# Kernel optimization log

Measured on AMD Instinct MI355X. Metric: run time of the kernel, lower is better.

## Reference

```python
import jax, jax.numpy as jnp
import numpy as np

B, S, D = 4, 2048, 1024
H, HD = 16, 64  # n_heads, head_dim (n_kv_heads == n_heads -> n_rep = 1)
WINDOW = 256
ROPE_THETA = 10000.0


def setup_inputs() -> dict:
    key = jax.random.key(0)
    ks = jax.random.split(key, 5)
    x = jax.random.normal(ks[0], (B, S, D), dtype=jnp.float32)
    scale = 0.02
    wq = jax.random.normal(ks[1], (D, D), dtype=jnp.float32) * scale
    wk = jax.random.normal(ks[2], (D, D), dtype=jnp.float32) * scale
    wv = jax.random.normal(ks[3], (D, D), dtype=jnp.float32) * scale
    wo = jax.random.normal(ks[4], (D, D), dtype=jnp.float32) * scale
    # RoPE frequencies: freqs_cis[t, i] = exp(1j * t / theta^(2i/HD)), i in [0, HD/2)
    inv_freq = 1.0 / (ROPE_THETA ** (jnp.arange(0, HD, 2, dtype=jnp.float32) / HD))
    t = jnp.arange(S, dtype=jnp.float32)
    ang = t[:, None] * inv_freq[None, :]  # [S, HD/2]
    return {"x": x, "freqs_cos": jnp.cos(ang), "freqs_sin": jnp.sin(ang),
            "wq": wq, "wk": wk, "wv": wv, "wo": wo}


def _apply_rope(xq, xk, cos, sin):
    # xq/xk: [B, S, H, HD]; cos/sin: [S, HD/2] broadcast as [1, S, 1, HD/2]
    def rot(v):
        vr = v.reshape(*v.shape[:-1], HD // 2, 2)
        v0, v1 = vr[..., 0], vr[..., 1]
        c = cos[None, :, None, :]
        s = sin[None, :, None, :]
        o0 = v0 * c - v1 * s
        o1 = v0 * s + v1 * c
        return jnp.stack([o0, o1], axis=-1).reshape(v.shape)
    return rot(xq), rot(xk)


def reference(x, freqs_cos, freqs_sin, wq, wk, wv, wo):
    b, s, _ = x.shape
    xq = (x @ wq.T).reshape(b, s, H, HD)
    xk = (x @ wk.T).reshape(b, s, H, HD)
    xv = (x @ wv.T).reshape(b, s, H, HD)
    xq, xk = _apply_rope(xq, xk, freqs_cos, freqs_sin)
    # [B, H, S, S] scores
    scores = jnp.einsum('bqhd,bkhd->bhqk', xq, xk) / jnp.sqrt(jnp.float32(HD))
    pos = jnp.arange(s)
    # masked (disallowed) when j > i (future) or i - j >= window
    bad = (pos[None, :] > pos[:, None]) | (pos[:, None] - pos[None, :] >= WINDOW)
    scores = jnp.where(bad[None, None], -jnp.inf, scores)
    attn = jax.nn.softmax(scores.astype(jnp.float32), axis=-1).astype(xq.dtype)
    out = jnp.einsum('bhqk,bkhd->bqhd', attn, xv).reshape(b, s, H * HD)
    return out @ wo.T
```

## Files before the change

kernel.cpp:

```cpp
#include <hip/hip_runtime.h>
#include <hip/hip_bf16.h>


typedef __bf16 bf16_t;
typedef __attribute__((ext_vector_type(8))) __bf16 bf16x8;
typedef __attribute__((ext_vector_type(4))) __bf16 bf16x4;
typedef __attribute__((ext_vector_type(4))) float f32x4;

#define MFMA16(a, b, c) __builtin_amdgcn_mfma_f32_16x16x32_bf16((a), (b), (c), 0, 0, 0)

__device__ __forceinline__ void async16(const void* g, void* l) {
    __builtin_amdgcn_global_load_lds(
        (const __attribute__((address_space(1))) unsigned int*)g,
        (__attribute__((address_space(3))) unsigned int*)l, 16, 0, 0);
}

#define BAR() do { asm volatile("" ::: "memory"); __builtin_amdgcn_s_barrier(); \
                   asm volatile("" ::: "memory"); } while (0)
#define VMC(N) asm volatile("s_waitcnt vmcnt(" #N ")" ::: "memory")
#define LGKM0() asm volatile("s_waitcnt lgkmcnt(0)" ::: "memory")

__global__ __launch_bounds__(256) void cvt_all(const float* __restrict__ x,
                                               const float* __restrict__ wq,
                                               const float* __restrict__ wk,
                                               const float* __restrict__ wv,
                                               const float* __restrict__ wo,
                                               const float* __restrict__ fcos,
                                               const float* __restrict__ fsin,
                                               bf16_t* __restrict__ xbf,
                                               bf16_t* __restrict__ wqkv,
                                               bf16_t* __restrict__ wobf,
                                               float* __restrict__ fcosT,
                                               float* __restrict__ fsinT) {
    const int blk = blockIdx.x;
    if (blk >= 6144) {
        const int p = blk - 6144;
        for (int s = threadIdx.x; s < 2048; s += 256) {
            fcosT[p * 2048 + s] = fcos[s * 32 + p];
            fsinT[p * 2048 + s] = fsin[s * 32 + p];
        }
        return;
    }
    const float* s;
    bf16_t* d;
    int base;
    if (blk < 4096)      { s = x;  d = xbf;            base = blk; }
    else if (blk < 4608) { s = wq; d = wqkv;           base = blk - 4096; }
    else if (blk < 5120) { s = wk; d = wqkv + 1048576; base = blk - 4608; }
    else if (blk < 5632) { s = wv; d = wqkv + 2097152; base = blk - 5120; }
    else                 { s = wo; d = wobf;           base = blk - 5632; }
    const int i = (base * 256 + threadIdx.x) * 8;
    float4 a = *(const float4*)(s + i);
    float4 b = *(const float4*)(s + i + 4);
    bf16x8 o;
    o[0] = (bf16_t)a.x; o[1] = (bf16_t)a.y; o[2] = (bf16_t)a.z; o[3] = (bf16_t)a.w;
    o[4] = (bf16_t)b.x; o[5] = (bf16_t)b.y; o[6] = (bf16_t)b.z; o[7] = (bf16_t)b.w;
    *(bf16x8*)(d + i) = o;
}

__global__ __launch_bounds__(512, 1) __attribute__((amdgpu_waves_per_eu(2)))
void gemm192_qkv(const bf16_t* __restrict__ A, const bf16_t* __restrict__ Bw,
                 const float* __restrict__ fcosT, const float* __restrict__ fsinT,
                 bf16_t* __restrict__ Qo, bf16_t* __restrict__ Ko,
                 bf16_t* __restrict__ VT, int M, int N, int K) {
    __shared__ __attribute__((aligned(16))) bf16_t As[32768];
    __shared__ __attribute__((aligned(16))) bf16_t Bs[24576];
    const int tid = threadIdx.x;
    const int l = tid & 63, w = tid >> 6;
    const int lr = l & 15, lg = l >> 4;
    const int wr = w >> 2, wc = w & 3;

    const int nwg = gridDim.x * gridDim.y;
    const int flat = blockIdx.y * gridDim.x + blockIdx.x;
    const int swz = (flat & 7) * (nwg >> 3) + (flat >> 3);
    const int bx = swz % gridDim.x, by = swz / gridDim.x;
    const long m0 = (long)by * 256, n0 = (long)bx * 192;
    const int NT = K >> 6;
    const int NI = NT >> 1;

    const int p  = w * 1024 + l * 16;
    const int pp = p ^ (((p >> 9) & 1) << 5);
    const int st = pp >> 10;
    const int rSt = (st >> 1) * 16 + ((pp >> 6) & 15);
    const int cSt = (st & 1) * 32 + ((pp >> 4) & 3) * 8;
    const bf16_t* aS = A  + (m0 + rSt) * K + cSt;
    const bf16_t* bS = Bw + (n0 + rSt) * K + cSt;
    const long uK = 64L * K;

    auto stageA = [&](int b, int u, int t) {
        async16(aS + (long)u * uK + (long)t * 64,
                (char*)As + b * 32768 + u * 8192 + w * 1024);
    };
    auto stageB = [&](int b, int u, int t) {
        async16(bS + (long)u * uK + (long)t * 64,
                (char*)Bs + b * 24576 + u * 8192 + w * 1024);
    };

    f32x4 acc[8][3] = {};
    bf16x8 afX[4], afY[4], bfX[3], bfY[3];
    const int swd = (lr & 8) << 2;

    auto loadAF = [&](int b, int mh, int ks, bf16x8 (&dst)[4]) {
#pragma unroll
        for (int mi = 0; mi < 4; ++mi) {
            const int off = (wr * 2 + mh) * 8192 + (mi * 2 + ks) * 1024 +
                            lr * 64 + lg * 16;
            dst[mi] = *(const bf16x8*)((const char*)As + b * 32768 + (off ^ swd));
        }
    };
    auto loadBF = [&](int b, int ks, bf16x8 (&dst)[3]) {
#pragma unroll
        for (int nj = 0; nj < 3; ++nj) {
            const int rg = wc * 48 + nj * 16 + lr;
            const int off = (rg >> 6) * 8192 + (((rg >> 4) & 3) * 2 + ks) * 1024 +
                            lr * 64 + lg * 16;
            dst[nj] = *(const bf16x8*)((const char*)Bs + b * 24576 + (off ^ swd));
        }
    };

#define QMM(MH, AF, BF) do {                                                   \
    __builtin_amdgcn_s_setprio(1);                                             \
    _Pragma("unroll")                                                          \
    for (int mi = 0; mi < 4; ++mi)                                             \
        _Pragma("unroll")                                                      \
        for (int nj = 0; nj < 3; ++nj)                                         \
            acc[(MH)*4+mi][nj] = MFMA16((AF)[mi], (BF)[nj], acc[(MH)*4+mi][nj]); \
    __builtin_amdgcn_s_setprio(0);                                             \
} while (0)

    stageA(0, 0, 0); stageA(0, 1, 0); stageA(0, 2, 0); stageA(0, 3, 0);
    stageB(0, 0, 0); stageB(0, 1, 0); stageB(0, 2, 0);
    stageB(1, 0, 1); stageB(1, 1, 1); stageB(1, 2, 1);
    VMC(3);
    BAR();

#pragma unroll 1
    for (int it = 0; it < NI - 1; ++it) {
        const int T = 2 * it;
        loadAF(0, 0, 0, afX); loadBF(0, 0, bfX);
        stageA(1, 0, T + 1); stageA(1, 1, T + 1);
        BAR(); QMM(0, afX, bfX); BAR();
        loadAF(0, 1, 0, afY);
        stageA(1, 2, T + 1); stageA(1, 3, T + 1);
        BAR(); QMM(1, afY, bfX); BAR();
        loadAF(0, 0, 1, afX); loadBF(0, 1, bfY);
        BAR(); QMM(0, afX, bfY); BAR();
        loadAF(0, 1, 1, afY);
        stageB(0, 0, T + 2);
        BAR(); QMM(1, afY, bfY); VMC(1); BAR();
        loadAF(1, 0, 0, afX); loadBF(1, 0, bfX);
        stageB(0, 1, T + 2); stageB(0, 2, T + 2);
        BAR(); QMM(0, afX, bfX); BAR();
        loadAF(1, 1, 0, afY);
        stageA(0, 0, T + 2); stageA(0, 1, T + 2);
        BAR(); QMM(1, afY, bfX); BAR();
        loadAF(1, 0, 1, afX); loadBF(1, 1, bfY);
        stageA(0, 2, T + 2); stageA(0, 3, T + 2);
        BAR(); QMM(0, afX, bfY); BAR();
        loadAF(1, 1, 1, afY);
        stageB(1, 0, T + 3); stageB(1, 1, T + 3); stageB(1, 2, T + 3);
        BAR(); QMM(1, afY, bfY); VMC(3); BAR();
    }

    {
        loadAF(0, 0, 0, afX); loadBF(0, 0, bfX);
        stageA(1, 0, NT - 1); stageA(1, 1, NT - 1);
        BAR(); QMM(0, afX, bfX); BAR();
        loadAF(0, 1, 0, afY);
        stageA(1, 2, NT - 1); stageA(1, 3, NT - 1);
        BAR(); QMM(1, afY, bfX); BAR();
        loadAF(0, 0, 1, afX); loadBF(0, 1, bfY);
        BAR(); QMM(0, afX, bfY); BAR();
        loadAF(0, 1, 1, afY);
        BAR(); QMM(1, afY, bfY);
        VMC(0); BAR();
        loadAF(1, 0, 0, afX); loadBF(1, 0, bfX);
        QMM(0, afX, bfX);
        loadAF(1, 1, 0, afY);
        QMM(1, afY, bfX);
        loadAF(1, 0, 1, afX); loadBF(1, 1, bfY);
        QMM(0, afX, bfY);
        loadAF(1, 1, 1, afY);
        QMM(1, afY, bfY);
    }
#undef QMM

    bf16_t* scr = (w < 6) ? (bf16_t*)((char*)As + w * 4608)
                          : (bf16_t*)((char*)Bs + (w - 6) * 4608);
    asm volatile("" ::: "memory");

#pragma unroll
    for (int nj = 0; nj < 3; ++nj) {
        const int cbase = (int)n0 + wc * 48 + nj * 16;
        const int cls = cbase >> 10;
        if (cls == 2) {
#pragma unroll
            for (int ai = 0; ai < 8; ++ai)
#pragma unroll
                for (int j = 0; j < 4; ++j)
                    scr[(ai * 16 + lg * 4 + j) * 18 + lr] = (bf16_t)acc[ai][nj][j];
            LGKM0();
            asm volatile("" ::: "memory");
            const int ch = l & 15;
            const int g0 = l >> 4;
            const int d16 = cbase - 2048 + ch;
            const int hh = d16 >> 6, dd = d16 & 63;
            const long T0 = m0 + wr * 128;
            const int bb = (int)(T0 >> 11);
            const int s0 = (int)(T0 & 2047);
            bf16_t* vrow = VT + ((long)((bb * 16 + hh) * 64 + dd) * 2048) + s0;
#pragma unroll
            for (int qq = 0; qq < 4; ++qq) {
                const int grp = g0 + qq * 4;
                bf16x8 o;
#pragma unroll
                for (int j = 0; j < 8; ++j) {
                    const int f = ((j & 3) << 1) | (j >> 2);
                    o[j] = scr[(grp * 8 + f) * 18 + ch];
                }
                *(bf16x8*)(vrow + grp * 8) = o;
            }
            LGKM0();
            asm volatile("" ::: "memory");
        } else {
            const int c = cbase + lr;
            const int dd = c & 63;
            const int p2 = dd >> 1;
            const int hh = (c >> 6) & 15;
            const float sgn = (lr & 1) ? 1.f : -1.f;
            bf16_t* qk = (cls == 0) ? Qo : Ko;
            const float* cT = fcosT + p2 * 2048;
            const float* sT = fsinT + p2 * 2048;
#pragma unroll
            for (int ai = 0; ai < 8; ++ai) {
                const long t0 = m0 + wr * 128 + ai * 16 + lg * 4;
                const int s0 = (int)(t0 & 2047);
                const int bb = (int)(t0 >> 11);
                const float4 cc = *(const float4*)(cT + s0);
                const float4 ss = *(const float4*)(sT + s0);
                bf16_t* row = qk + ((long)(bb * 16 + hh) * 2048 + s0) * 64 + dd;
                const float v0 = acc[ai][nj][0], pv0 = __shfl_xor(acc[ai][nj][0], 1);
                const float v1 = acc[ai][nj][1], pv1 = __shfl_xor(acc[ai][nj][1], 1);
                const float v2 = acc[ai][nj][2], pv2 = __shfl_xor(acc[ai][nj][2], 1);
                const float v3 = acc[ai][nj][3], pv3 = __shfl_xor(acc[ai][nj][3], 1);
                row[0]       = (bf16_t)(v0 * cc.x + sgn * (pv0 * ss.x));
                row[64]      = (bf16_t)(v1 * cc.y + sgn * (pv1 * ss.y));
                row[128]     = (bf16_t)(v2 * cc.z + sgn * (pv2 * ss.z));
                row[192]     = (bf16_t)(v3 * cc.w + sgn * (pv3 * ss.w));
            }
        }
    }
}

template <typename OUT>
__global__ __launch_bounds__(512, 2) void gemm256(const bf16_t* __restrict__ A,
                                                  const bf16_t* __restrict__ Bw,
                                                  OUT* __restrict__ C,
                                                  int M, int N, int K) {
    __shared__ __attribute__((aligned(16))) bf16_t As[49152];
    __shared__ __attribute__((aligned(16))) bf16_t Bs[24576];
    const int tid = threadIdx.x;
    const int l = tid & 63, w = tid >> 6;
    const int lr = l & 15, lg = l >> 4;
    const int wr = w >> 1, wc = w & 1;

    const int nwg = gridDim.x * gridDim.y;
    const int flat = blockIdx.y * gridDim.x + blockIdx.x;
    const int swz = (flat & 7) * (nwg >> 3) + (flat >> 3);
    const int bx = swz % gridDim.x, by = swz / gridDim.x;
    const long m0 = (long)by * 256, n0 = (long)bx * 128;
    const int NT = K >> 6;

    int rS[2], cS[2];
#pragma unroll
    for (int i = 0; i < 2; ++i) {
        const int p  = i * 8192 + w * 1024 + l * 16;
        const int pp = p ^ (((p >> 9) & 1) << 5);
        const int st = pp >> 10;
        rS[i] = (st >> 1) * 16 + ((pp >> 6) & 15);
        cS[i] = (st & 1) * 32 + ((pp >> 4) & 3) * 8;
    }
    const bf16_t* aSrc0 = A  + (m0 + rS[0]) * K + cS[0];
    const bf16_t* aSrc1 = A  + (m0 + rS[1]) * K + cS[1];
    const bf16_t* bSrc0 = Bw + (n0 + rS[0]) * K + cS[0];
    const bf16_t* bSrc1 = Bw + (n0 + rS[1]) * K + cS[1];
    const long hK = 128L * K;

    auto stageA = [&](int b, int h, int t) {
        char* d = (char*)As + b * 32768 + h * 16384 + w * 1024;
        const long o = (long)h * hK + (long)t * 64;
        async16(aSrc0 + o, d);
        async16(aSrc1 + o, d + 8192);
    };
    auto stageB = [&](int b, int t) {
        char* d = (char*)Bs + b * 16384 + w * 1024;
        const long o = (long)t * 64;
        async16(bSrc0 + o, d);
        async16(bSrc1 + o, d + 8192);
    };

    f32x4 acc[4][4] = {};
    bf16x8 af[4][2], blo[2][2], bhi[2][2];
    const int swd = (lr & 8) << 2;

    auto loadA = [&](int b) {
#pragma unroll
        for (int mi = 0; mi < 4; ++mi)
#pragma unroll
            for (int ks = 0; ks < 2; ++ks) {
                const int ra = (wr & 1) * 64 + mi * 16 + lr;
                const int off = ((ra >> 4) * 2 + ks) * 1024 + (ra & 15) * 64 + lg * 16;
                af[mi][ks] = *(const bf16x8*)((const char*)As + b * 32768 +
                                              (wr >> 1) * 16384 + (off ^ swd));
            }
    };
    auto loadB = [&](int b, int nh, bf16x8 (&dst)[2][2]) {
#pragma unroll
        for (int nj = 0; nj < 2; ++nj)
#pragma unroll
            for (int ks = 0; ks < 2; ++ks) {
                const int rb = wc * 64 + (nh * 2 + nj) * 16 + lr;
                const int off = ((rb >> 4) * 2 + ks) * 1024 + (rb & 15) * 64 + lg * 16;
                dst[nj][ks] = *(const bf16x8*)((const char*)Bs + b * 16384 +
                                               (off ^ swd));
            }
    };

#define QMM(NH, BF) do {                                                       \
    __builtin_amdgcn_s_setprio(1);                                             \
    _Pragma("unroll")                                                          \
    for (int mi = 0; mi < 4; ++mi) {                                           \
        acc[mi][(NH)*2]   = MFMA16(af[mi][0], (BF)[0][0], acc[mi][(NH)*2]);    \
        acc[mi][(NH)*2]   = MFMA16(af[mi][1], (BF)[0][1], acc[mi][(NH)*2]);    \
        acc[mi][(NH)*2+1] = MFMA16(af[mi][0], (BF)[1][0], acc[mi][(NH)*2+1]);  \
        acc[mi][(NH)*2+1] = MFMA16(af[mi][1], (BF)[1][1], acc[mi][(NH)*2+1]);  \
    }                                                                          \
    __builtin_amdgcn_s_setprio(0);                                             \
} while (0)

    stageA(0, 0, 0); stageA(0, 1, 0); stageB(0, 0);
    stageA(1, 0, 1); stageA(1, 1, 1); stageB(1, 1);
    VMC(6);
    BAR();

    int bc = 0;
#pragma unroll 1
    for (int t = 0; t < NT - 2; ++t) {
        const int bn = (bc + 2 >= 3) ? bc - 1 : bc + 2;
        loadA(bc); loadB(bc, 0, blo); stageA(bn, 0, t + 2); stageA(bn, 1, t + 2);
        BAR(); QMM(0, blo); BAR();
        loadB(bc, 1, bhi); stageB(bn, t + 2);
        BAR(); QMM(1, bhi);
        if (t < NT - 3) { VMC(6); } else { VMC(0); }
        BAR();
        bc = (bc + 1 >= 3) ? 0 : bc + 1;
    }
    {
        loadA(bc); loadB(bc, 0, blo);
        QMM(0, blo);
        loadB(bc, 1, bhi);
        QMM(1, bhi);
        const int b2 = (bc + 1 >= 3) ? 0 : bc + 1;
        loadA(b2); loadB(b2, 0, blo);
        QMM(0, blo);
        loadB(b2, 1, bhi);
        QMM(1, bhi);
    }
#undef QMM

#pragma unroll
    for (int mi = 0; mi < 4; ++mi)
#pragma unroll
        for (int ni = 0; ni < 4; ++ni)
#pragma unroll
            for (int j = 0; j < 4; ++j) {
                long r = m0 + wr * 64 + mi * 16 + lg * 4 + j;
                long c = n0 + wc * 64 + ni * 16 + lr;
                C[r * N + c] = (OUT)acc[mi][ni][j];
            }
}

__global__ __launch_bounds__(256, 2) void attn_win4(const bf16_t* __restrict__ Q,
                                                    const bf16_t* __restrict__ Kb,
                                                    const bf16_t* __restrict__ VT,
                                                    bf16_t* __restrict__ Ao) {
    __shared__ __attribute__((aligned(16))) bf16_t kld[5 * 4096];
    __shared__ __attribute__((aligned(16))) bf16_t vld[5 * 4096];
    const int raw = blockIdx.x;
    const int mswz = ((raw & 7) << 8) | (raw >> 3);
    const int qt = mswz & 31, bh = mswz >> 5;
    const int h = bh & 15, b = bh >> 4;
    const int l = threadIdx.x & 63, w = threadIdx.x >> 6;
    const int lr = l & 15, lg = l >> 4;
    const int q0 = qt * 64 + w * 16;
    const int q = q0 + lr;
    const int tb = qt - 4;

    const bf16_t* Qp = Q + (long)bh * 2048 * 64;
    const bf16_t* Kp = Kb + (long)bh * 2048 * 64;
    const bf16_t* Vp = VT + (long)bh * 64 * 2048;

#pragma unroll
    for (int u = 0; u < 5; ++u) {
        const int kt = tb + u;
        const int kt64 = (kt < 0 ? 0 : kt) * 64;
#pragma unroll
        for (int part = 0; part < 2; ++part) {
            const int seg = w * 2 + part;
            const int r = seg * 8 + (l >> 3);
            const int sc = (l & 7) ^ ((r >> 1) & 7);
            async16(Kp + (long)(kt64 + r) * 64 + sc * 8,
                    (char*)kld + u * 8192 + seg * 1024);
            async16(Vp + (long)r * 2048 + kt64 + sc * 8,
                    (char*)vld + u * 8192 + seg * 1024);
        }
    }

    const bf16x8 qb0 = *(const bf16x8*)&Qp[q * 64 + lg * 8];
    const bf16x8 qb1 = *(const bf16x8*)&Qp[q * 64 + 32 + lg * 8];

    __syncthreads();

    float mrun = -1000.f, lsum = 0.f;
    f32x4 o0 = {0.f, 0.f, 0.f, 0.f}, o1 = {0.f, 0.f, 0.f, 0.f};
    f32x4 o2 = {0.f, 0.f, 0.f, 0.f}, o3 = {0.f, 0.f, 0.f, 0.f};
    const int swv = (lr >> 1) & 7;

    const char* kbase;
    const char* vbase;
    int k0s;

#define QKCORE(HH, MM)                                                           \
        const int row_ = (HH) * 32 + 2 * lr + (MM);                              \
        const int sw_ = (row_ >> 1) & 7;                                         \
        bf16x8 k0_ = *(const bf16x8*)(kbase + row_ * 128 + ((lg ^ sw_) << 4));   \
        bf16x8 k1_ = *(const bf16x8*)(kbase + row_ * 128 + (((4 + lg) ^ sw_) << 4)); \
        f32x4 s_ = {0.f, 0.f, 0.f, 0.f};                                         \
        s_ = MFMA16(k0_, qb0, s_);                                               \
        s_ = MFMA16(k1_, qb1, s_);

#define QKF_F(DST, HH, MM)                                                       \
    f32x4 DST; { QKCORE(HH, MM)                                                  \
        const int kb_ = k0s + (HH) * 32 + (MM) + lg * 8;                         \
        DST[0] = ((kb_ >= 0) & ((unsigned)(q - kb_) < 256u))         ? s_[0] * 0.125f : -1e30f; \
        DST[1] = ((kb_ + 2 >= 0) & ((unsigned)(q - kb_ - 2) < 256u)) ? s_[1] * 0.125f : -1e30f; \
        DST[2] = ((kb_ + 4 >= 0) & ((unsigned)(q - kb_ - 4) < 256u)) ? s_[2] * 0.125f : -1e30f; \
        DST[3] = ((kb_ + 6 >= 0) & ((unsigned)(q - kb_ - 6) < 256u)) ? s_[3] * 0.125f : -1e30f; \
    }

#define QKF_U(DST, HH, MM)                                                       \
    f32x4 DST; { QKCORE(HH, MM)                                                  \
        const int d_ = q - (k0s + (HH) * 32 + (MM) + lg * 8);                    \
        DST[0] = (d_ < 256)     ? s_[0] * 0.125f : -1e30f;                       \
        DST[1] = (d_ - 2 < 256) ? s_[1] * 0.125f : -1e30f;                       \
        DST[2] = (d_ - 4 < 256) ? s_[2] * 0.125f : -1e30f;                       \
        DST[3] = (d_ - 6 < 256) ? s_[3] * 0.125f : -1e30f;                       \
    }

#define QKF_L(DST, HH, MM)                                                       \
    f32x4 DST; { QKCORE(HH, MM)                                                  \
        const int d_ = q - (k0s + (HH) * 32 + (MM) + lg * 8);                    \
        DST[0] = (d_ >= 0)     ? s_[0] * 0.125f : -1e30f;                        \
        DST[1] = (d_ - 2 >= 0) ? s_[1] * 0.125f : -1e30f;                        \
        DST[2] = (d_ - 4 >= 0) ? s_[2] * 0.125f : -1e30f;                        \
        DST[3] = (d_ - 6 >= 0) ? s_[3] * 0.125f : -1e30f;                        \
    }

#define QKF_N(DST, HH, MM)                                                       \
    f32x4 DST; { QKCORE(HH, MM)                                                  \
        DST[0] = s_[0] * 0.125f; DST[1] = s_[1] * 0.125f;                        \
        DST[2] = s_[2] * 0.125f; DST[3] = s_[3] * 0.125f;                        \
    }

#define EXV(S_) {                                                                \
        S_[0] = __expf(S_[0] - mnew); S_[1] = __expf(S_[1] - mnew);              \
        S_[2] = __expf(S_[2] - mnew); S_[3] = __expf(S_[3] - mnew);              \
        rs += (S_[0] + S_[1]) + (S_[2] + S_[3]); }

#define PVF(NT, HH, PB) {                                                        \
        bf16x8 va_ = *(const bf16x8*)(vbase + ((NT) * 16 + lr) * 128 +           \
                                      ((((HH) * 4 + lg) ^ swv) << 4));           \
        o##NT = MFMA16(va_, PB, o##NT); }

#define TILEBODY(QKM) {                                                          \
        QKM(sA, 0, 0) QKM(sB, 0, 1) QKM(sC, 1, 0) QKM(sD, 1, 1)                  \
        float tm = fmaxf(fmaxf(fmaxf(sA[0], sA[1]), fmaxf(sA[2], sA[3])),        \
                         fmaxf(fmaxf(sB[0], sB[1]), fmaxf(sB[2], sB[3])));       \
        tm = fmaxf(tm, fmaxf(fmaxf(fmaxf(sC[0], sC[1]), fmaxf(sC[2], sC[3])),    \
                             fmaxf(fmaxf(sD[0], sD[1]), fmaxf(sD[2], sD[3]))));  \
        tm = fmaxf(tm, __shfl_xor(tm, 16));                                      \
        tm = fmaxf(tm, __shfl_xor(tm, 32));                                      \
        const float mnew = fmaxf(mrun, tm);                                      \
        const float alpha = __expf(mrun - mnew);                                 \
        mrun = mnew;                                                             \
        float rs = 0.f;                                                          \
        EXV(sA) EXV(sB) EXV(sC) EXV(sD)                                          \
        rs += __shfl_xor(rs, 16);                                                \
        rs += __shfl_xor(rs, 32);                                                \
        lsum = lsum * alpha + rs;                                                \
        o0[0] *= alpha; o0[1] *= alpha; o0[2] *= alpha; o0[3] *= alpha;          \
        o1[0] *= alpha; o1[1] *= alpha; o1[2] *= alpha; o1[3] *= alpha;          \
        o2[0] *= alpha; o2[1] *= alpha; o2[2] *= alpha; o2[3] *= alpha;          \
        o3[0] *= alpha; o3[1] *= alpha; o3[2] *= alpha; o3[3] *= alpha;          \
        bf16x8 pb0, pb1;                                                         \
        pb0[0] = (bf16_t)sA[0]; pb0[1] = (bf16_t)sA[1]; pb0[2] = (bf16_t)sA[2]; pb0[3] = (bf16_t)sA[3]; \
        pb0[4] = (bf16_t)sB[0]; pb0[5] = (bf16_t)sB[1]; pb0[6] = (bf16_t)sB[2]; pb0[7] = (bf16_t)sB[3]; \
        pb1[0] = (bf16_t)sC[0]; pb1[1] = (bf16_t)sC[1]; pb1[2] = (bf16_t)sC[2]; pb1[3] = (bf16_t)sC[3]; \
        pb1[4] = (bf16_t)sD[0]; pb1[5] = (bf16_t)sD[1]; pb1[6] = (bf16_t)sD[2]; pb1[7] = (bf16_t)sD[3]; \
        PVF(0, 0, pb0) PVF(1, 0, pb0) PVF(2, 0, pb0) PVF(3, 0, pb0)              \
        PVF(0, 1, pb1) PVF(1, 1, pb1) PVF(2, 1, pb1) PVF(3, 1, pb1)              \
    }

#define SETT(U) kbase = (const char*)kld + (U) * 8192;                           \
                vbase = (const char*)vld + (U) * 8192;                           \
                k0s = (tb + (U)) * 64;

    if (qt >= 4) {
        SETT(0) TILEBODY(QKF_U)
        SETT(1) TILEBODY(QKF_N)
        SETT(2) TILEBODY(QKF_N)
        SETT(3) TILEBODY(QKF_N)
        SETT(4) TILEBODY(QKF_L)
    } else {
#pragma unroll
        for (int u = 0; u < 5; ++u) {
            SETT(u) TILEBODY(QKF_F)
        }
    }
#undef SETT
#undef TILEBODY
#undef QKF_F
#undef QKF_U
#undef QKF_L
#undef QKF_N
#undef QKCORE
#undef EXV
#undef PVF

    const float rinv = 1.0f / lsum;
    bf16_t* aor = Ao + ((long)(b * 2048) + q) * 1024 + h * 64;
#define EPI(NT, OA_) {                                                           \
        bf16x4 ov_;                                                             \
        ov_[0] = (bf16_t)(OA_[0] * rinv); ov_[1] = (bf16_t)(OA_[1] * rinv);      \
        ov_[2] = (bf16_t)(OA_[2] * rinv); ov_[3] = (bf16_t)(OA_[3] * rinv);      \
        *(bf16x4*)(aor + (NT) * 16 + lg * 4) = ov_; }
    EPI(0, o0) EPI(1, o1) EPI(2, o2) EPI(3, o3)
#undef EPI
}

extern "C" void kernel_launch(void* const* d_in, const int* in_sizes, int n_in,
                              void* d_out, int out_size, void* d_ws, size_t ws_size,
                              hipStream_t stream) {
    (void)in_sizes; (void)n_in; (void)out_size; (void)ws_size;
    const float* x    = (const float*)d_in[0];
    const float* fcos = (const float*)d_in[1];
    const float* fsin = (const float*)d_in[2];
    const float* wq   = (const float*)d_in[3];
    const float* wk   = (const float*)d_in[4];
    const float* wv   = (const float*)d_in[5];
    const float* wo   = (const float*)d_in[6];
    float* out = (float*)d_out;

    char* ws = (char*)d_ws;
    bf16_t* xbf   = (bf16_t*)(ws);
    bf16_t* wqkv  = (bf16_t*)(ws + 16777216);
    bf16_t* wobf  = (bf16_t*)(ws + 23068672);
    float*  fcosT = (float*)(ws + 25165824);
    float*  fsinT = (float*)(ws + 25427968);
    bf16_t* qbuf  = (bf16_t*)(ws + 41943040);
    bf16_t* kbuf  = (bf16_t*)(ws + 75497472);
    bf16_t* vtb   = (bf16_t*)(ws + 92274688);
    bf16_t* aob   = xbf;

    cvt_all<<<6176, 256, 0, stream>>>(x, wq, wk, wv, wo, fcos, fsin,
                                      xbf, wqkv, wobf, fcosT, fsinT);

    gemm192_qkv<<<dim3(16, 32), 512, 0, stream>>>(xbf, wqkv, fcosT, fsinT,
                                                  qbuf, kbuf, vtb,
                                                  8192, 3072, 1024);
    attn_win4<<<2048, 256, 0, stream>>>(qbuf, kbuf, vtb, aob);
    gemm256<float><<<dim3(8, 32), 512, 0, stream>>>(aob, wobf, out, 8192, 1024, 1024);
}
```

Measured before the change: 126.9 us.

## Read V directly from global in attention, fold softmax scale into Q, raise occupancy

The attention kernel no longer stages V tiles in LDS; each PV MFMA operand is loaded straight from global VT memory, halving shared memory so launch bounds can request 4 blocks per SM. The 1/sqrt(HD) scale is folded into Q during the RoPE epilogue of the projection GEMM, removing per-score multiplies. The V-transpose scatter in the projection epilogue is remapped so each lane group writes contiguous 8-element chunks along the sequence. The trade-off is uncached-by-LDS global V reads with latency exposed in the inner loop, and bf16 rounding of pre-scaled Q.

```diff
diff --git a/kernel.cpp b/kernel.cpp
--- a/kernel.cpp
+++ b/kernel.cpp
@@ -201,8 +201,8 @@
                     scr[(ai * 16 + lg * 4 + j) * 18 + lr] = (bf16_t)acc[ai][nj][j];
             LGKM0();
             asm volatile("" ::: "memory");
-            const int ch = l & 15;
-            const int g0 = l >> 4;
+            const int ch = l >> 2;
+            const int sub = l & 3;
             const int d16 = cbase - 2048 + ch;
             const int hh = d16 >> 6, dd = d16 & 63;
             const long T0 = m0 + wr * 128;
@@ -211,14 +211,14 @@
             bf16_t* vrow = VT + ((long)((bb * 16 + hh) * 64 + dd) * 2048) + s0;
 #pragma unroll
             for (int qq = 0; qq < 4; ++qq) {
-                const int grp = g0 + qq * 4;
+                const int tb8 = qq * 32 + sub * 8;
                 bf16x8 o;
 #pragma unroll
                 for (int j = 0; j < 8; ++j) {
                     const int f = ((j & 3) << 1) | (j >> 2);
-                    o[j] = scr[(grp * 8 + f) * 18 + ch];
+                    o[j] = scr[(tb8 + f) * 18 + ch];
                 }
-                *(bf16x8*)(vrow + grp * 8) = o;
+                *(bf16x8*)(vrow + tb8) = o;
             }
             LGKM0();
             asm volatile("" ::: "memory");
@@ -228,6 +228,7 @@
             const int p2 = dd >> 1;
             const int hh = (c >> 6) & 15;
             const float sgn = (lr & 1) ? 1.f : -1.f;
+            const float sc = (cls == 0) ? 0.125f : 1.f;
             bf16_t* qk = (cls == 0) ? Qo : Ko;
             const float* cT = fcosT + p2 * 2048;
             const float* sT = fsinT + p2 * 2048;
@@ -243,10 +244,10 @@
                 const float v1 = acc[ai][nj][1], pv1 = __shfl_xor(acc[ai][nj][1], 1);
                 const float v2 = acc[ai][nj][2], pv2 = __shfl_xor(acc[ai][nj][2], 1);
                 const float v3 = acc[ai][nj][3], pv3 = __shfl_xor(acc[ai][nj][3], 1);
-                row[0]       = (bf16_t)(v0 * cc.x + sgn * (pv0 * ss.x));
-                row[64]      = (bf16_t)(v1 * cc.y + sgn * (pv1 * ss.y));
-                row[128]     = (bf16_t)(v2 * cc.z + sgn * (pv2 * ss.z));
-                row[192]     = (bf16_t)(v3 * cc.w + sgn * (pv3 * ss.w));
+                row[0]   = (bf16_t)((v0 * cc.x + sgn * (pv0 * ss.x)) * sc);
+                row[64]  = (bf16_t)((v1 * cc.y + sgn * (pv1 * ss.y)) * sc);
+                row[128] = (bf16_t)((v2 * cc.z + sgn * (pv2 * ss.z)) * sc);
+                row[192] = (bf16_t)((v3 * cc.w + sgn * (pv3 * ss.w)) * sc);
             }
         }
     }
@@ -380,12 +381,11 @@
             }
 }
 
-__global__ __launch_bounds__(256, 2) void attn_win4(const bf16_t* __restrict__ Q,
+__global__ __launch_bounds__(256, 4) void attn_win4(const bf16_t* __restrict__ Q,
                                                     const bf16_t* __restrict__ Kb,
                                                     const bf16_t* __restrict__ VT,
                                                     bf16_t* __restrict__ Ao) {
     __shared__ __attribute__((aligned(16))) bf16_t kld[5 * 4096];
-    __shared__ __attribute__((aligned(16))) bf16_t vld[5 * 4096];
     const int raw = blockIdx.x;
     const int mswz = ((raw & 7) << 8) | (raw >> 3);
     const int qt = mswz & 31, bh = mswz >> 5;
@@ -411,8 +411,6 @@
             const int sc = (l & 7) ^ ((r >> 1) & 7);
             async16(Kp + (long)(kt64 + r) * 64 + sc * 8,
                     (char*)kld + u * 8192 + seg * 1024);
-            async16(Vp + (long)r * 2048 + kt64 + sc * 8,
-                    (char*)vld + u * 8192 + seg * 1024);
         }
     }
 
@@ -424,11 +422,9 @@
     float mrun = -1000.f, lsum = 0.f;
     f32x4 o0 = {0.f, 0.f, 0.f, 0.f}, o1 = {0.f, 0.f, 0.f, 0.f};
     f32x4 o2 = {0.f, 0.f, 0.f, 0.f}, o3 = {0.f, 0.f, 0.f, 0.f};
-    const int swv = (lr >> 1) & 7;
 
     const char* kbase;
-    const char* vbase;
-    int k0s;
+    int k0s, kt64c;
 
 #define QKCORE(HH, MM)                                                           \
         const int row_ = (HH) * 32 + 2 * lr + (MM);                              \
@@ -442,34 +438,33 @@
 #define QKF_F(DST, HH, MM)                                                       \
     f32x4 DST; { QKCORE(HH, MM)                                                  \
         const int kb_ = k0s + (HH) * 32 + (MM) + lg * 8;                         \
-        DST[0] = ((kb_ >= 0) & ((unsigned)(q - kb_) < 256u))         ? s_[0] * 0.125f : -1e30f; \
-        DST[1] = ((kb_ + 2 >= 0) & ((unsigned)(q - kb_ - 2) < 256u)) ? s_[1] * 0.125f : -1e30f; \
-        DST[2] = ((kb_ + 4 >= 0) & ((unsigned)(q - kb_ - 4) < 256u)) ? s_[2] * 0.125f : -1e30f; \
-        DST[3] = ((kb_ + 6 >= 0) & ((unsigned)(q - kb_ - 6) < 256u)) ? s_[3] * 0.125f : -1e30f; \
+        DST[0] = ((kb_ >= 0) & ((unsigned)(q - kb_) < 256u))         ? s_[0] : -1e30f; \
+        DST[1] = ((kb_ + 2 >= 0) & ((unsigned)(q - kb_ - 2) < 256u)) ? s_[1] : -1e30f; \
+        DST[2] = ((kb_ + 4 >= 0) & ((unsigned)(q - kb_ - 4) < 256u)) ? s_[2] : -1e30f; \
+        DST[3] = ((kb_ + 6 >= 0) & ((unsigned)(q - kb_ - 6) < 256u)) ? s_[3] : -1e30f; \
     }
 
 #define QKF_U(DST, HH, MM)                                                       \
     f32x4 DST; { QKCORE(HH, MM)                                                  \
         const int d_ = q - (k0s + (HH) * 32 + (MM) + lg * 8);                    \
-        DST[0] = (d_ < 256)     ? s_[0] * 0.125f : -1e30f;                       \
-        DST[1] = (d_ - 2 < 256) ? s_[1] * 0.125f : -1e30f;                       \
-        DST[2] = (d_ - 4 < 256) ? s_[2] * 0.125f : -1e30f;                       \
-        DST[3] = (d_ - 6 < 256) ? s_[3] * 0.125f : -1e30f;                       \
+        DST[0] = (d_ < 256)     ? s_[0] : -1e30f;                                \
+        DST[1] = (d_ - 2 < 256) ? s_[1] : -1e30f;                                \
+        DST[2] = (d_ - 4 < 256) ? s_[2] : -1e30f;                                \
+        DST[3] = (d_ - 6 < 256) ? s_[3] : -1e30f;                                \
     }
 
 #define QKF_L(DST, HH, MM)                                                       \
     f32x4 DST; { QKCORE(HH, MM)                                                  \
         const int d_ = q - (k0s + (HH) * 32 + (MM) + lg * 8);                    \
-        DST[0] = (d_ >= 0)     ? s_[0] * 0.125f : -1e30f;                        \
-        DST[1] = (d_ - 2 >= 0) ? s_[1] * 0.125f : -1e30f;                        \
-        DST[2] = (d_ - 4 >= 0) ? s_[2] * 0.125f : -1e30f;                        \
-        DST[3] = (d_ - 6 >= 0) ? s_[3] * 0.125f : -1e30f;                        \
+        DST[0] = (d_ >= 0)     ? s_[0] : -1e30f;                                 \
+        DST[1] = (d_ - 2 >= 0) ? s_[1] : -1e30f;                                 \
+        DST[2] = (d_ - 4 >= 0) ? s_[2] : -1e30f;                                 \
+        DST[3] = (d_ - 6 >= 0) ? s_[3] : -1e30f;                                 \
     }
 
 #define QKF_N(DST, HH, MM)                                                       \
     f32x4 DST; { QKCORE(HH, MM)                                                  \
-        DST[0] = s_[0] * 0.125f; DST[1] = s_[1] * 0.125f;                        \
-        DST[2] = s_[2] * 0.125f; DST[3] = s_[3] * 0.125f;                        \
+        DST[0] = s_[0]; DST[1] = s_[1]; DST[2] = s_[2]; DST[3] = s_[3];          \
     }
 
 #define EXV(S_) {                                                                \
@@ -478,8 +473,8 @@
         rs += (S_[0] + S_[1]) + (S_[2] + S_[3]); }
 
 #define PVF(NT, HH, PB) {                                                        \
-        bf16x8 va_ = *(const bf16x8*)(vbase + ((NT) * 16 + lr) * 128 +           \
-                                      ((((HH) * 4 + lg) ^ swv) << 4));           \
+        bf16x8 va_ = *(const bf16x8*)(Vp + (long)((NT) * 16 + lr) * 2048 +       \
+                                      kt64c + ((HH) * 4 + lg) * 8);              \
         o##NT = MFMA16(va_, PB, o##NT); }
 
 #define TILEBODY(QKM) {                                                          \
@@ -512,8 +507,8 @@
     }
 
 #define SETT(U) kbase = (const char*)kld + (U) * 8192;                           \
-                vbase = (const char*)vld + (U) * 8192;                           \
-                k0s = (tb + (U)) * 64;
+                k0s = (tb + (U)) * 64;                                           \
+                kt64c = (tb + (U) < 0 ? 0 : tb + (U)) * 64;
 
     if (qt >= 4) {
         SETT(0) TILEBODY(QKF_U)
```

After: 147.5 us. 16.3% more time.
